# Kernel tuning notes

Measured on AMD Instinct MI355X. Metric: run time of the kernel, lower is better.

Reference implementation:

```python
import jax, jax.numpy as jnp
import numpy as np

IGST = 10      # ghost-cell width (module-level constant in the source)
EPS = 0.01     # tol passed to NeuralODE -> runge_kutta eps
W_SCALE = 0.05 # keep the learned stencil contractive over 100 steps


def cal_boundry(u):
    # Replace the IGST ghost cells on each side with the nearest interior value.
    m, n, l = u.shape
    left = jnp.broadcast_to(u[:, :, IGST:IGST + 1], (m, n, IGST))
    right = jnp.broadcast_to(u[:, :, -IGST - 1:-IGST], (m, n, IGST))
    return jnp.concatenate([left, u[:, :, IGST:-IGST], right], axis=2)


def stencil_f(z, W):
    # func: learned 1D stencil = same-padded conv over the spatial axis.
    # z: [m, n, l], W: [n_out, n_in, k]
    return jax.lax.conv_general_dilated(
        z, W, window_strides=(1,), padding='SAME',
        dimension_numbers=('NCH', 'OIH', 'NCH'))


def setup_inputs() -> dict:
    key = jax.random.key(0)
    k1, k2 = jax.random.split(key)
    z0 = jax.random.normal(k1, (32, 16, 8192), dtype=jnp.float32)
    W = jax.random.normal(k2, (16, 16, 5), dtype=jnp.float32) * W_SCALE
    return {'z0': z0, 'W': W, 't1_t0': 1}


def reference(z0, W, t1_t0):
    # SSP-RK3 (Shu-Osher) explicit time stepping with ghost-cell BCs.
    n_steps = int(round(t1_t0 / EPS))
    h = t1_t0 / n_steps

    def step(z, _):
        k1 = cal_boundry(z + h * stencil_f(z, W))
        k2 = cal_boundry(0.75 * z + 0.25 * k1 + 0.25 * h * stencil_f(k1, W))
        z_new = cal_boundry(z / 3.0 + 2.0 * k2 / 3.0 + 2.0 * h * stencil_f(k2, W) / 3.0)
        return z_new, None

    z, _ = jax.lax.scan(step, z0, None, length=n_steps)
    return z
```

## Files before the change

kernel.cpp:

```cpp
#include <hip/hip_runtime.h>


#define NCH    16
#define LL     8192
#define TX     128
#define NBX    64
#define NB     32
#define NSTEPS 100
#define SPK    5
#define NKER   (NSTEPS / SPK)

#define RAD    30
#define NCHUNK 31
#define ISLAB  190

#define WCOLS  96
#define DWIN   1072
#define NROWS  592
#define NMT    37
#define NKC    34
#define XSTR   1096

typedef __bf16 bf16x8 __attribute__((ext_vector_type(8)));
typedef __bf16 bf16x4 __attribute__((ext_vector_type(4)));
typedef float  f32x4  __attribute__((ext_vector_type(4)));

__device__ __align__(16) float g_G [ 5*256];
__device__ __align__(16) float g_G2[ 9*256];
__device__ __align__(16) float g_Tp[13*256];
__device__ __align__(16) float g_T2[25*256];
__device__ __align__(16) float g_T3[37*256];
__device__ __align__(16) float g_T4[49*256];
__device__ __align__(16) float g_T5[61*256];
__device__ __align__(16) __bf16 g_Sfrag[NCHUNK*64*8];
__device__ __align__(16) float g_CL[(size_t)NROWS*DWIN];
__device__ __align__(16) float g_CR[(size_t)NROWS*DWIN];
__device__ __align__(16) __bf16 g_Cpack[2][NMT][NKC][512];

__global__ void build_G(const float* __restrict__ W, const int* __restrict__ tptr) {
  const float h = (float)(*tptr) / (float)NSTEPS;
  const int o = threadIdx.x >> 4, i = threadIdx.x & 15;
#pragma unroll
  for (int k = 0; k < 5; ++k)
    g_G[k*256 + o*16 + i] = h * W[o*80 + i*5 + k];
}

__global__ void compose_k(int mode) {
  const float* A; int ra; const float* B; int rb; float* C;
  switch (mode) {
    case 0:  A = g_G;  ra = 2;  B = g_G;  rb = 2; C = g_G2; break;
    case 1:  A = g_G2; ra = 4;  B = g_G;  rb = 2; C = g_Tp; break;
    case 2:  A = g_Tp; ra = 6;  B = g_Tp; rb = 6; C = g_T2; break;
    case 3:  A = g_T2; ra = 12; B = g_Tp; rb = 6; C = g_T3; break;
    case 4:  A = g_T3; ra = 18; B = g_Tp; rb = 6; C = g_T4; break;
    default: A = g_T4; ra = 24; B = g_Tp; rb = 6; C = g_T5; break;
  }
  const int rc = ra + rb;
  const int d = (int)blockIdx.x - rc;
  const int o = threadIdx.x >> 4, i = threadIdx.x & 15;
  float acc = 0.f;
  for (int a = -ra; a <= ra; ++a) {
    const int b = d - a;
    if (b < -rb || b > rb) continue;
    const float* Am = A + (a+ra)*256 + o*16;
    const float* Bm = B + (b+rb)*256 + i;
#pragma unroll
    for (int j = 0; j < 16; ++j) acc += Am[j] * Bm[j*16];
  }
  C[(size_t)blockIdx.x*256 + o*16 + i] = acc;
}

__global__ void build_Tp() {
  const int o = threadIdx.x >> 4, i = threadIdx.x & 15;
#pragma unroll
  for (int k = 0; k < 13; ++k) {
    const int d = k - 6;
    float v = g_Tp[k*256 + o*16 + i] * (1.f/6.f);
    if (d >= -4 && d <= 4) v += 0.5f * g_G2[(d+4)*256 + o*16 + i];
    if (d >= -2 && d <= 2) v += g_G[(d+2)*256 + o*16 + i];
    g_Tp[k*256 + o*16 + i] = v;
  }
}

__device__ __forceinline__ float padread(const float* M, int r, int d, int oi) {
  return (d >= -r && d <= r) ? M[(d+r)*256 + oi] : 0.f;
}

__global__ void pack_S() {
  const int c = blockIdx.x;
  const int lane = threadIdx.x & 63;
  const int jj = (threadIdx.x >> 6) * 2;
  const int gg = lane >> 4, n = lane & 15;
  const int k = 2*c + (gg >> 1);
  const int d = k - RAD;
#pragma unroll
  for (int u = 0; u < 2; ++u) {
    const int j = jj + u;
    const int i = (gg & 1)*8 + j;
    const int oi = n*16 + i;
    float v = 0.f;
    if (k <= 60) {
      v = 5.f  * padread(g_Tp,  6, d, oi)
        + 10.f * padread(g_T2, 12, d, oi)
        + 10.f * padread(g_T3, 18, d, oi)
        + 5.f  * padread(g_T4, 24, d, oi)
        +        padread(g_T5, 30, d, oi);
    }
    g_Sfrag[((size_t)c*64 + lane)*8 + j] = (__bf16)v;
  }
}

__global__ void pack_C() {
  const int mt = blockIdx.x, e = blockIdx.y;
  const float* __restrict__ C = e ? g_CR : g_CL;
  __bf16* __restrict__ P = &g_Cpack[e][mt][0][0];
  for (int idx = threadIdx.x; idx < NKC * 512; idx += 256) {
    const int kc = idx >> 9, q = idx & 511;
    const int ln = q >> 3, j = q & 7;
    const int k = kc * 32 + (ln >> 4) * 8 + j;
    const int row = mt * 16 + (ln & 15);
    P[idx] = (__bf16)((k < DWIN) ? C[(size_t)row * DWIN + k] : 0.f);
  }
}

__device__ __forceinline__ int ldsIdx(int col, int ch) {
  return col * NCH + (ch ^ ((col & 4) << 1));
}

__device__ __forceinline__ bf16x8 mkA(const float* __restrict__ W, int c, int g, int n) {
  const int kk = c * 2 + (g >> 1);
  bf16x8 a;
#pragma unroll
  for (int j = 0; j < 8; ++j) {
    const int i = (g & 1) * 8 + j;
    a[j] = (__bf16)((kk < 5) ? W[n * (NCH * 5) + i * 5 + kk] : 0.0f);
  }
  return a;
}

__global__ __launch_bounds__(384)
void edge_evolve(const float* __restrict__ W, const int* __restrict__ tptr) {
  __shared__ __align__(16) __bf16 ES[2][WCOLS * NCH];
  const int j = blockIdx.x, e = blockIdx.y;
  const float h = (float)(*tptr) / (float)NSTEPS;
  const int tid = threadIdx.x, lane = tid & 63, wv = tid >> 6;
  const int g = lane >> 4, n = lane & 15;
  const int t = wv, mycol = 16 * t + n;
  const int cwj = (e ? 29 : 0) + (j >> 4), chj = j & 15;

  const bf16x8 af0 = mkA(W, 0, g, n);
  const bf16x8 af1 = mkA(W, 1, g, n);
  const bf16x8 af2 = mkA(W, 2, g, n);

  const int hot = ldsIdx(cwj, chj);
  for (int q = tid; q < WCOLS * NCH; q += 384)
    ES[0][q] = (__bf16)(q == hot ? 1.f : 0.f);

  f32x4 kz = {0.f, 0.f, 0.f, 0.f};
  if (mycol == cwj && g == (chj >> 2)) kz[chj & 3] = 1.f;
  f32x4 kf = {0.f, 0.f, 0.f, 0.f};
  __syncthreads();

  const float c13 = 1.0f / 3.0f, c23 = 2.0f / 3.0f;
  int rb = 0;
#pragma unroll 1
  for (int sp = 0; sp < SPK; ++sp) {
#pragma unroll 1
    for (int st = 0; st < 3; ++st) {
      const float az  = (st == 0) ? 1.0f : (st == 1) ? 0.75f : c13;
      const float ak  = (st == 0) ? 0.0f : (st == 1) ? 0.25f : c23;
      const float agh = (st == 0) ? h    : (st == 1) ? 0.25f*h : c23*h;
      const __bf16* RS = ES[rb];
      __bf16* WS = ES[rb ^ 1];
      f32x4 acc = {0.f, 0.f, 0.f, 0.f};
#pragma unroll
      for (int c = 0; c < 3; ++c) {
        const int kk = c * 2 + (g >> 1);
        int s = mycol + kk - 2;
        s = min(max(s, 0), WCOLS - 1);
        const bf16x8 bfrag = *(const bf16x8*)(&RS[ldsIdx(s, (g & 1) * 8)]);
        const bf16x8 a = (c == 0) ? af0 : (c == 1) ? af1 : af2;
        acc = __builtin_amdgcn_mfma_f32_16x16x32_bf16(a, bfrag, acc, 0, 0, 0);
      }
      f32x4 v;
#pragma unroll
      for (int r = 0; r < 4; ++r) v[r] = az * kz[r] + ak * kf[r] + agh * acc[r];
      if (e == 0 && t == 0) {
#pragma unroll
        for (int r = 0; r < 4; ++r) {
          const float sv = __shfl(v[r], (lane & 48) | 10, 64);
          if (n < 10) v[r] = sv;
        }
      }
      if (e == 1 && t == 5) {
#pragma unroll
        for (int r = 0; r < 4; ++r) {
          const float sv = __shfl(v[r], (lane & 48) | 5, 64);
          if (n > 5) v[r] = sv;
        }
      }
      kf = v;
      if (st == 2) kz = v;
      bf16x4 bv = { (__bf16)v[0], (__bf16)v[1], (__bf16)v[2], (__bf16)v[3] };
      *(bf16x4*)(&WS[ldsIdx(mycol, g * 4)]) = bv;
      __syncthreads();
      rb ^= 1;
    }
  }

  if (e == 0) {
    if (mycol <= 36) {
      const int rowb = mycol * 16 + g * 4;
#pragma unroll
      for (int r = 0; r < 4; ++r) {
        const float id = (mycol == cwj && (g * 4 + r) == chj) ? 1.f : 0.f;
        g_CL[(size_t)(rowb + r) * DWIN + j] = kz[r] - id;
      }
    }
  } else {
    if (mycol >= 59) {
      const int rowb = (mycol - 59) * 16 + g * 4;
#pragma unroll
      for (int r = 0; r < 4; ++r) {
        const float id = (mycol == cwj && (g * 4 + r) == chj) ? 1.f : 0.f;
        g_CR[(size_t)(rowb + r) * DWIN + j] = kz[r] - id;
      }
    }
  }
}

__global__ __launch_bounds__(256) void transpose_kernel(const float* __restrict__ in,
                                                        float* __restrict__ out) {
  const int b = blockIdx.y;
  const int x = blockIdx.x * 256 + threadIdx.x;
  const float* __restrict__ ib = in + (size_t)b * NCH * LL;
  float* __restrict__ ob = out + (size_t)b * NCH * LL;
  float v[NCH];
#pragma unroll
  for (int c = 0; c < NCH; ++c) v[c] = ib[c * LL + x];
#pragma unroll
  for (int c = 0; c < NCH; c += 4)
    *(float4*)(ob + (size_t)x * NCH + c) = make_float4(v[c], v[c+1], v[c+2], v[c+3]);
}

__global__ __launch_bounds__(256)
void multistep_kernel(
    const float* __restrict__ zin,
    float* __restrict__ zout,
    const int* __restrict__ tptr, int finalKer)
{
  __shared__ __align__(16) char SMEM[16 * XSTR * 2];

  const int b = blockIdx.y, bx = blockIdx.x;
  const int tid = threadIdx.x, lane = tid & 63, wv = tid >> 6;
  const int g = lane >> 4, n = lane & 15;

  if (bx < NBX) {
    __bf16* __restrict__ ISL = (__bf16*)SMEM;
    const float* __restrict__ zb = zin + (size_t)b * NCH * LL;
    float* __restrict__ ob = zout + (size_t)b * NCH * LL;
    const int x0 = bx * TX;
    const bool leftE = (bx == 0), rightE = (bx == NBX - 1);

    for (int q = tid; q < ISLAB * 4; q += 256) {
      const int s = q >> 2, cg = (q & 3) * 4;
      int gx = x0 - RAD + s;
      gx = min(max(gx, 0), LL - 1);
      const float4 v = *(const float4*)(zb + (size_t)gx * NCH + cg);
      bf16x4 bv = { (__bf16)v.x, (__bf16)v.y, (__bf16)v.z, (__bf16)v.w };
      *(bf16x4*)(&ISL[ldsIdx(s, cg)]) = bv;
    }

    const int o0 = 16 * wv + n;
    const f32x4 kz0 = *(const f32x4*)(zb + (size_t)(x0 + o0) * NCH + g * 4);
    const f32x4 kz1 = *(const f32x4*)(zb + (size_t)(x0 + o0 + 64) * NCH + g * 4);
    __syncthreads();

    const int p = g >> 1, hsel = g & 1;
    f32x4 acc0 = {0.f,0.f,0.f,0.f}, acc1 = acc0;
    const __bf16* Af = g_Sfrag + (size_t)lane * 8;
    int col0 = o0 + p;
#pragma unroll
    for (int c = 0; c < NCHUNK; ++c) {
      const bf16x8 a = *(const bf16x8*)(Af + (size_t)c * 512);
      const int xr = ((((col0 >> 2) & 1) ^ hsel) << 4);
      const bf16x8 b0 = *(const bf16x8*)((const char*)ISL + col0 * 32 + xr);
      const bf16x8 b1 = *(const bf16x8*)((const char*)ISL + (col0 + 64) * 32 + xr);
      acc0 = __builtin_amdgcn_mfma_f32_16x16x32_bf16(a, b0, acc0, 0, 0, 0);
      acc1 = __builtin_amdgcn_mfma_f32_16x16x32_bf16(a, b1, acc1, 0, 0, 0);
      col0 += 2;
    }

    f32x4 v0, v1;
#pragma unroll
    for (int r = 0; r < 4; ++r) { v0[r] = kz0[r] + acc0[r]; v1[r] = kz1[r] + acc1[r]; }

    const bool st0 = !(leftE && o0 <= 36);
    const bool st1 = !(rightE && o0 >= 27);
    if (!finalKer) {
      if (st0) *(f32x4*)(ob + (size_t)(x0 + o0) * NCH + g * 4) = v0;
      if (st1) *(f32x4*)(ob + (size_t)(x0 + o0 + 64) * NCH + g * 4) = v1;
    } else {
#pragma unroll
      for (int r = 0; r < 4; ++r) {
        if (st0) ob[(size_t)(g * 4 + r) * LL + (x0 + o0)] = v0[r];
        if (st1) ob[(size_t)(g * 4 + r) * LL + (x0 + o0 + 64)] = v1[r];
      }
    }
  } else {
    const int rid = b;
    const int side = rid & 1, bhalf = (rid >> 1) & 1, mseg = rid >> 2;
    __bf16* __restrict__ XL = (__bf16*)SMEM;
    const size_t woff = side ? (size_t)(LL - 67) * NCH : 0;

    for (int q = tid; q < 16 * 268; q += 256) {
      const int bb = q / 268, c4 = q % 268;
      const f32x4 v = *(const f32x4*)(zin + (size_t)(bhalf*16 + bb) * NCH * LL
                                      + woff + c4 * 4);
      bf16x4 bv = { (__bf16)v[0], (__bf16)v[1], (__bf16)v[2], (__bf16)v[3] };
      *(bf16x4*)(&XL[bb * XSTR + c4 * 4]) = bv;
    }
    for (int q = tid; q < 16 * 16; q += 256)
      XL[(q >> 4) * XSTR + 1072 + (q & 15)] = (__bf16)0.f;
    __syncthreads();

    const int q = mseg * 4 + wv;
    const int mt0 = q, mt1 = q + 32;
    const bool has1 = (mt1 < NMT);
    f32x4 acc0 = {0.f,0.f,0.f,0.f}, acc1 = acc0;
    const __bf16* __restrict__ Cp = &g_Cpack[side][0][0][0];
    const __bf16* __restrict__ Xr = &XL[n * XSTR + g * 8];

#pragma unroll 2
    for (int kc = 0; kc < NKC; ++kc) {
      const bf16x8 a = *(const bf16x8*)(Xr + kc * 32);
      const bf16x8 b0 = *(const bf16x8*)(Cp + ((size_t)mt0 * NKC + kc) * 512 + lane * 8);
      acc0 = __builtin_amdgcn_mfma_f32_16x16x32_bf16(a, b0, acc0, 0, 0, 0);
      if (has1) {
        const bf16x8 b1 = *(const bf16x8*)(Cp + ((size_t)mt1 * NKC + kc) * 512 + lane * 8);
        acc1 = __builtin_amdgcn_mfma_f32_16x16x32_bf16(a, b1, acc1, 0, 0, 0);
      }
    }

#pragma unroll
    for (int i = 0; i < 2; ++i) {
      if (i == 1 && !has1) break;
      const int mt = i ? mt1 : mt0;
      const f32x4 acc = i ? acc1 : acc0;
      const int x = side ? (LL - 37 + mt) : mt;
#pragma unroll
      for (int r = 0; r < 4; ++r) {
        const int bb = bhalf * 16 + 4 * g + r;
        const size_t base = (size_t)bb * NCH * LL;
        const float ov = zin[base + (size_t)x * NCH + n] + acc[r];
        if (!finalKer) zout[base + (size_t)x * NCH + n] = ov;
        else           zout[base + (size_t)n * LL + x] = ov;
      }
    }
  }
}

extern "C" void kernel_launch(void* const* d_in, const int* in_sizes, int n_in,
                              void* d_out, int out_size, void* d_ws, size_t ws_size,
                              hipStream_t stream) {
  const float* z0 = (const float*)d_in[0];
  const float* W  = (const float*)d_in[1];
  const int*   t  = (const int*)d_in[2];

  float* Q = (float*)d_out;
  float* P = (float*)d_ws;

  build_G<<<dim3(1), dim3(256), 0, stream>>>(W, t);
  compose_k<<<dim3( 9), dim3(256), 0, stream>>>(0);
  compose_k<<<dim3(13), dim3(256), 0, stream>>>(1);
  build_Tp<<<dim3(1), dim3(256), 0, stream>>>();
  compose_k<<<dim3(25), dim3(256), 0, stream>>>(2);
  compose_k<<<dim3(37), dim3(256), 0, stream>>>(3);
  compose_k<<<dim3(49), dim3(256), 0, stream>>>(4);
  compose_k<<<dim3(61), dim3(256), 0, stream>>>(5);
  pack_S<<<dim3(NCHUNK), dim3(256), 0, stream>>>();

  edge_evolve<<<dim3(DWIN, 2), dim3(384), 0, stream>>>(W, t);
  pack_C<<<dim3(NMT, 2), dim3(256), 0, stream>>>();

  dim3 block(256);
  transpose_kernel<<<dim3(32, NB), block, 0, stream>>>(z0, Q);

  dim3 mgrid(NBX + 1, NB);
  for (int k = 1; k <= NKER; ++k) {
    if (k & 1) multistep_kernel<<<mgrid, block, 0, stream>>>(Q, P, t, 0);
    else       multistep_kernel<<<mgrid, block, 0, stream>>>(P, Q, t, k == NKER);
  }
}
```

Baseline: 789.2 us.

## Fuse setup kernels, single-wave edge evolve, split boundary blocks finer

Merges the chain of small stencil-composition and packing kernels into one 1024-thread block, removing eight launches and their serialization. Rewrites edge_evolve to use one wavefront per block that loops over six column tiles, keeping kz/kf state in LDS so no block barriers are needed. Splits the boundary-correction work of the multistep kernel across an extra grid column with 8-batch groups, which halves LDS per block and spreads the edge GEMM over more blocks. In exchange, half of each MFMA's A rows are zero-padded, so those lanes do wasted work.

```diff
diff --git a/kernel.cpp b/kernel.cpp
--- a/kernel.cpp
+++ b/kernel.cpp
@@ -37,48 +37,23 @@
 __device__ __align__(16) float g_CR[(size_t)NROWS*DWIN];
 __device__ __align__(16) __bf16 g_Cpack[2][NMT][NKC][512];
 
-__global__ void build_G(const float* __restrict__ W, const int* __restrict__ tptr) {
-  const float h = (float)(*tptr) / (float)NSTEPS;
-  const int o = threadIdx.x >> 4, i = threadIdx.x & 15;
-#pragma unroll
-  for (int k = 0; k < 5; ++k)
-    g_G[k*256 + o*16 + i] = h * W[o*80 + i*5 + k];
-}
-
-__global__ void compose_k(int mode) {
-  const float* A; int ra; const float* B; int rb; float* C;
-  switch (mode) {
-    case 0:  A = g_G;  ra = 2;  B = g_G;  rb = 2; C = g_G2; break;
-    case 1:  A = g_G2; ra = 4;  B = g_G;  rb = 2; C = g_Tp; break;
-    case 2:  A = g_Tp; ra = 6;  B = g_Tp; rb = 6; C = g_T2; break;
-    case 3:  A = g_T2; ra = 12; B = g_Tp; rb = 6; C = g_T3; break;
-    case 4:  A = g_T3; ra = 18; B = g_Tp; rb = 6; C = g_T4; break;
-    default: A = g_T4; ra = 24; B = g_Tp; rb = 6; C = g_T5; break;
-  }
-  const int rc = ra + rb;
-  const int d = (int)blockIdx.x - rc;
-  const int o = threadIdx.x >> 4, i = threadIdx.x & 15;
-  float acc = 0.f;
-  for (int a = -ra; a <= ra; ++a) {
-    const int b = d - a;
-    if (b < -rb || b > rb) continue;
-    const float* Am = A + (a+ra)*256 + o*16;
-    const float* Bm = B + (b+rb)*256 + i;
-#pragma unroll
-    for (int j = 0; j < 16; ++j) acc += Am[j] * Bm[j*16];
-  }
-  C[(size_t)blockIdx.x*256 + o*16 + i] = acc;
-}
-
-__global__ void build_Tp() {
-  const int o = threadIdx.x >> 4, i = threadIdx.x & 15;
-#pragma unroll
-  for (int k = 0; k < 13; ++k) {
-    const int d = k - 6;
-    float v = g_Tp[k*256 + o*16 + i] * (1.f/6.f);
-    if (d >= -4 && d <= 4) v += 0.5f * g_G2[(d+4)*256 + o*16 + i];
-    if (d >= -2 && d <= 2) v += g_G[(d+2)*256 + o*16 + i];
-    g_Tp[k*256 + o*16 + i] = v;
+__device__ __forceinline__ void composeSeg(const float* __restrict__ A, int ra,
+                                           const float* __restrict__ B, int rb,
+                                           float* __restrict__ C, int q, int oi) {
+  const int o = oi >> 4, i = oi & 15;
+  const int rc = ra + rb, nt = 2*rc + 1;
+  for (int kt = q; kt < nt; kt += 4) {
+    const int d = kt - rc;
+    float acc = 0.f;
+    for (int a = -ra; a <= ra; ++a) {
+      const int b = d - a;
+      if (b < -rb || b > rb) continue;
+      const float* Am = A + (a+ra)*256 + o*16;
+      const float* Bm = B + (b+rb)*256 + i;
+#pragma unroll
+      for (int j = 0; j < 16; ++j) acc += Am[j] * Bm[j*16];
+    }
+    C[(size_t)kt*256 + oi] = acc;
   }
 }
 
@@ -86,25 +61,46 @@
   return (d >= -r && d <= r) ? M[(d+r)*256 + oi] : 0.f;
 }
 
-__global__ void pack_S() {
-  const int c = blockIdx.x;
-  const int lane = threadIdx.x & 63;
-  const int jj = (threadIdx.x >> 6) * 2;
-  const int gg = lane >> 4, n = lane & 15;
-  const int k = 2*c + (gg >> 1);
-  const int d = k - RAD;
-#pragma unroll
-  for (int u = 0; u < 2; ++u) {
-    const int j = jj + u;
-    const int i = (gg & 1)*8 + j;
-    const int oi = n*16 + i;
+__global__ __launch_bounds__(1024)
+void setup_S(const float* __restrict__ W, const int* __restrict__ tptr) {
+  const float h = (float)(*tptr) / (float)NSTEPS;
+  const int q = threadIdx.x >> 8;
+  const int oi = threadIdx.x & 255;
+  const int o = oi >> 4, i = oi & 15;
+
+  for (int k = q; k < 5; k += 4)
+    g_G[k*256 + oi] = h * W[o*80 + i*5 + k];
+  __syncthreads();
+  composeSeg(g_G,  2, g_G,  2, g_G2, q, oi);  __syncthreads();
+  composeSeg(g_G2, 4, g_G,  2, g_Tp, q, oi);  __syncthreads();
+  for (int k = q; k < 13; k += 4) {
+    const int d = k - 6;
+    float v = g_Tp[k*256 + oi] * (1.f/6.f);
+    if (d >= -4 && d <= 4) v += 0.5f * g_G2[(d+4)*256 + oi];
+    if (d >= -2 && d <= 2) v += g_G[(d+2)*256 + oi];
+    g_Tp[k*256 + oi] = v;
+  }
+  __syncthreads();
+  composeSeg(g_Tp, 6,  g_Tp, 6, g_T2, q, oi); __syncthreads();
+  composeSeg(g_T2, 12, g_Tp, 6, g_T3, q, oi); __syncthreads();
+  composeSeg(g_T3, 18, g_Tp, 6, g_T4, q, oi); __syncthreads();
+  composeSeg(g_T4, 24, g_Tp, 6, g_T5, q, oi); __syncthreads();
+
+  for (int idx = threadIdx.x; idx < NCHUNK*512; idx += 1024) {
+    const int c = idx >> 9, rest = idx & 511;
+    const int lane = rest >> 3, j = rest & 7;
+    const int gg = lane >> 4, n = lane & 15;
+    const int k = 2*c + (gg >> 1);
+    const int d = k - RAD;
+    const int ii = (gg & 1)*8 + j;
+    const int oi2 = n*16 + ii;
     float v = 0.f;
     if (k <= 60) {
-      v = 5.f  * padread(g_Tp,  6, d, oi)
-        + 10.f * padread(g_T2, 12, d, oi)
-        + 10.f * padread(g_T3, 18, d, oi)
-        + 5.f  * padread(g_T4, 24, d, oi)
-        +        padread(g_T5, 30, d, oi);
+      v = 5.f  * padread(g_Tp,  6, d, oi2)
+        + 10.f * padread(g_T2, 12, d, oi2)
+        + 10.f * padread(g_T3, 18, d, oi2)
+        + 5.f  * padread(g_T4, 24, d, oi2)
+        +        padread(g_T5, 30, d, oi2);
     }
     g_Sfrag[((size_t)c*64 + lane)*8 + j] = (__bf16)v;
   }
@@ -138,14 +134,15 @@
   return a;
 }
 
-__global__ __launch_bounds__(384)
+__global__ __launch_bounds__(64)
 void edge_evolve(const float* __restrict__ W, const int* __restrict__ tptr) {
   __shared__ __align__(16) __bf16 ES[2][WCOLS * NCH];
+  __shared__ __align__(16) float  KZ[WCOLS * NCH];
+  __shared__ __align__(16) float  KF[WCOLS * NCH];
   const int j = blockIdx.x, e = blockIdx.y;
   const float h = (float)(*tptr) / (float)NSTEPS;
-  const int tid = threadIdx.x, lane = tid & 63, wv = tid >> 6;
+  const int lane = threadIdx.x;
   const int g = lane >> 4, n = lane & 15;
-  const int t = wv, mycol = 16 * t + n;
   const int cwj = (e ? 29 : 0) + (j >> 4), chj = j & 15;
 
   const bf16x8 af0 = mkA(W, 0, g, n);
@@ -153,13 +150,12 @@
   const bf16x8 af2 = mkA(W, 2, g, n);
 
   const int hot = ldsIdx(cwj, chj);
-  for (int q = tid; q < WCOLS * NCH; q += 384)
+  const int hotz = cwj * 16 + chj;
+  for (int q = lane; q < WCOLS * NCH; q += 64) {
     ES[0][q] = (__bf16)(q == hot ? 1.f : 0.f);
-
-  f32x4 kz = {0.f, 0.f, 0.f, 0.f};
-  if (mycol == cwj && g == (chj >> 2)) kz[chj & 3] = 1.f;
-  f32x4 kf = {0.f, 0.f, 0.f, 0.f};
-  __syncthreads();
+    KZ[q] = (q == hotz) ? 1.f : 0.f;
+    KF[q] = 0.f;
+  }
 
   const float c13 = 1.0f / 3.0f, c23 = 2.0f / 3.0f;
   int rb = 0;
@@ -172,59 +168,58 @@
       const float agh = (st == 0) ? h    : (st == 1) ? 0.25f*h : c23*h;
       const __bf16* RS = ES[rb];
       __bf16* WS = ES[rb ^ 1];
-      f32x4 acc = {0.f, 0.f, 0.f, 0.f};
-#pragma unroll
-      for (int c = 0; c < 3; ++c) {
-        const int kk = c * 2 + (g >> 1);
-        int s = mycol + kk - 2;
-        s = min(max(s, 0), WCOLS - 1);
-        const bf16x8 bfrag = *(const bf16x8*)(&RS[ldsIdx(s, (g & 1) * 8)]);
-        const bf16x8 a = (c == 0) ? af0 : (c == 1) ? af1 : af2;
-        acc = __builtin_amdgcn_mfma_f32_16x16x32_bf16(a, bfrag, acc, 0, 0, 0);
-      }
-      f32x4 v;
-#pragma unroll
-      for (int r = 0; r < 4; ++r) v[r] = az * kz[r] + ak * kf[r] + agh * acc[r];
-      if (e == 0 && t == 0) {
-#pragma unroll
-        for (int r = 0; r < 4; ++r) {
-          const float sv = __shfl(v[r], (lane & 48) | 10, 64);
-          if (n < 10) v[r] = sv;
+#pragma unroll
+      for (int t = 0; t < 6; ++t) {
+        const int mycol = 16 * t + n;
+        const f32x4 kz = *(const f32x4*)(&KZ[mycol * 16 + g * 4]);
+        const f32x4 kf = *(const f32x4*)(&KF[mycol * 16 + g * 4]);
+        f32x4 acc = {0.f, 0.f, 0.f, 0.f};
+#pragma unroll
+        for (int c = 0; c < 3; ++c) {
+          const int kk = c * 2 + (g >> 1);
+          int s = mycol + kk - 2;
+          s = min(max(s, 0), WCOLS - 1);
+          const bf16x8 bfrag = *(const bf16x8*)(&RS[ldsIdx(s, (g & 1) * 8)]);
+          const bf16x8 a = (c == 0) ? af0 : (c == 1) ? af1 : af2;
+          acc = __builtin_amdgcn_mfma_f32_16x16x32_bf16(a, bfrag, acc, 0, 0, 0);
         }
-      }
-      if (e == 1 && t == 5) {
-#pragma unroll
-        for (int r = 0; r < 4; ++r) {
-          const float sv = __shfl(v[r], (lane & 48) | 5, 64);
-          if (n > 5) v[r] = sv;
+        f32x4 v;
+#pragma unroll
+        for (int r = 0; r < 4; ++r) v[r] = az * kz[r] + ak * kf[r] + agh * acc[r];
+        if (e == 0 && t == 0) {
+#pragma unroll
+          for (int r = 0; r < 4; ++r) {
+            const float sv = __shfl(v[r], (lane & 48) | 10, 64);
+            if (n < 10) v[r] = sv;
+          }
         }
-      }
-      kf = v;
-      if (st == 2) kz = v;
-      bf16x4 bv = { (__bf16)v[0], (__bf16)v[1], (__bf16)v[2], (__bf16)v[3] };
-      *(bf16x4*)(&WS[ldsIdx(mycol, g * 4)]) = bv;
-      __syncthreads();
+        if (e == 1 && t == 5) {
+#pragma unroll
+          for (int r = 0; r < 4; ++r) {
+            const float sv = __shfl(v[r], (lane & 48) | 5, 64);
+            if (n > 5) v[r] = sv;
+          }
+        }
+        *(f32x4*)(&KF[mycol * 16 + g * 4]) = v;
+        if (st == 2) *(f32x4*)(&KZ[mycol * 16 + g * 4]) = v;
+        bf16x4 bv = { (__bf16)v[0], (__bf16)v[1], (__bf16)v[2], (__bf16)v[3] };
+        *(bf16x4*)(&WS[ldsIdx(mycol, g * 4)]) = bv;
+      }
       rb ^= 1;
     }
   }
 
   if (e == 0) {
-    if (mycol <= 36) {
-      const int rowb = mycol * 16 + g * 4;
-#pragma unroll
-      for (int r = 0; r < 4; ++r) {
-        const float id = (mycol == cwj && (g * 4 + r) == chj) ? 1.f : 0.f;
-        g_CL[(size_t)(rowb + r) * DWIN + j] = kz[r] - id;
-      }
+    for (int idx = lane; idx < NROWS; idx += 64) {
+      const int col = idx >> 4, ch = idx & 15;
+      const float id = (col == cwj && ch == chj) ? 1.f : 0.f;
+      g_CL[(size_t)idx * DWIN + j] = KZ[col * 16 + ch] - id;
     }
   } else {
-    if (mycol >= 59) {
-      const int rowb = (mycol - 59) * 16 + g * 4;
-#pragma unroll
-      for (int r = 0; r < 4; ++r) {
-        const float id = (mycol == cwj && (g * 4 + r) == chj) ? 1.f : 0.f;
-        g_CR[(size_t)(rowb + r) * DWIN + j] = kz[r] - id;
-      }
+    for (int idx = lane; idx < NROWS; idx += 64) {
+      const int col = 59 + (idx >> 4), ch = idx & 15;
+      const float id = (col == cwj && ch == chj) ? 1.f : 0.f;
+      g_CR[(size_t)idx * DWIN + j] = KZ[col * 16 + ch] - id;
     }
   }
 }
@@ -249,7 +244,7 @@
     float* __restrict__ zout,
     const int* __restrict__ tptr, int finalKer)
 {
-  __shared__ __align__(16) char SMEM[16 * XSTR * 2];
+  __shared__ __align__(16) char SMEM[8 * XSTR * 2];
 
   const int b = blockIdx.y, bx = blockIdx.x;
   const int tid = threadIdx.x, lane = tid & 63, wv = tid >> 6;
@@ -308,32 +303,37 @@
       }
     }
   } else {
-    const int rid = b;
-    const int side = rid & 1, bhalf = (rid >> 1) & 1, mseg = rid >> 2;
+    const int rid = (bx - NBX) * NB + b;
+    const int side = rid & 1, bgroup = (rid >> 1) & 3, mseg = rid >> 3;
     __bf16* __restrict__ XL = (__bf16*)SMEM;
     const size_t woff = side ? (size_t)(LL - 67) * NCH : 0;
 
-    for (int q = tid; q < 16 * 268; q += 256) {
+    for (int q = tid; q < 8 * 268; q += 256) {
       const int bb = q / 268, c4 = q % 268;
-      const f32x4 v = *(const f32x4*)(zin + (size_t)(bhalf*16 + bb) * NCH * LL
+      const f32x4 v = *(const f32x4*)(zin + (size_t)(bgroup*8 + bb) * NCH * LL
                                       + woff + c4 * 4);
       bf16x4 bv = { (__bf16)v[0], (__bf16)v[1], (__bf16)v[2], (__bf16)v[3] };
       *(bf16x4*)(&XL[bb * XSTR + c4 * 4]) = bv;
     }
-    for (int q = tid; q < 16 * 16; q += 256)
-      XL[(q >> 4) * XSTR + 1072 + (q & 15)] = (__bf16)0.f;
+    if (tid < 8 * 24)
+      XL[(tid / 24) * XSTR + 1072 + (tid % 24)] = (__bf16)0.f;
     __syncthreads();
 
-    const int q = mseg * 4 + wv;
-    const int mt0 = q, mt1 = q + 32;
-    const bool has1 = (mt1 < NMT);
+    const int mt0 = mseg + 8 * wv;
+    const int mt1 = mseg + 32;
+    const bool has1 = (wv == 0 && mt1 < NMT);
     f32x4 acc0 = {0.f,0.f,0.f,0.f}, acc1 = acc0;
     const __bf16* __restrict__ Cp = &g_Cpack[side][0][0][0];
-    const __bf16* __restrict__ Xr = &XL[n * XSTR + g * 8];
+    const __bf16* __restrict__ Xr = &XL[(n & 7) * XSTR + g * 8];
 
 #pragma unroll 2
     for (int kc = 0; kc < NKC; ++kc) {
-      const bf16x8 a = *(const bf16x8*)(Xr + kc * 32);
+      bf16x8 a;
+      if (n < 8) a = *(const bf16x8*)(Xr + kc * 32);
+      else {
+#pragma unroll
+        for (int j = 0; j < 8; ++j) a[j] = (__bf16)0.f;
+      }
       const bf16x8 b0 = *(const bf16x8*)(Cp + ((size_t)mt0 * NKC + kc) * 512 + lane * 8);
       acc0 = __builtin_amdgcn_mfma_f32_16x16x32_bf16(a, b0, acc0, 0, 0, 0);
       if (has1) {
@@ -348,13 +348,15 @@
       const int mt = i ? mt1 : mt0;
       const f32x4 acc = i ? acc1 : acc0;
       const int x = side ? (LL - 37 + mt) : mt;
-#pragma unroll
-      for (int r = 0; r < 4; ++r) {
-        const int bb = bhalf * 16 + 4 * g + r;
-        const size_t base = (size_t)bb * NCH * LL;
-        const float ov = zin[base + (size_t)x * NCH + n] + acc[r];
-        if (!finalKer) zout[base + (size_t)x * NCH + n] = ov;
-        else           zout[base + (size_t)n * LL + x] = ov;
+      if (g < 2) {
+#pragma unroll
+        for (int r = 0; r < 4; ++r) {
+          const int bb = bgroup * 8 + 4 * g + r;
+          const size_t base = (size_t)bb * NCH * LL;
+          const float ov = zin[base + (size_t)x * NCH + n] + acc[r];
+          if (!finalKer) zout[base + (size_t)x * NCH + n] = ov;
+          else           zout[base + (size_t)n * LL + x] = ov;
+        }
       }
     }
   }
@@ -370,23 +372,14 @@
   float* Q = (float*)d_out;
   float* P = (float*)d_ws;
 
-  build_G<<<dim3(1), dim3(256), 0, stream>>>(W, t);
-  compose_k<<<dim3( 9), dim3(256), 0, stream>>>(0);
-  compose_k<<<dim3(13), dim3(256), 0, stream>>>(1);
-  build_Tp<<<dim3(1), dim3(256), 0, stream>>>();
-  compose_k<<<dim3(25), dim3(256), 0, stream>>>(2);
-  compose_k<<<dim3(37), dim3(256), 0, stream>>>(3);
-  compose_k<<<dim3(49), dim3(256), 0, stream>>>(4);
-  compose_k<<<dim3(61), dim3(256), 0, stream>>>(5);
-  pack_S<<<dim3(NCHUNK), dim3(256), 0, stream>>>();
-
-  edge_evolve<<<dim3(DWIN, 2), dim3(384), 0, stream>>>(W, t);
+  setup_S<<<dim3(1), dim3(1024), 0, stream>>>(W, t);
+  edge_evolve<<<dim3(DWIN, 2), dim3(64), 0, stream>>>(W, t);
   pack_C<<<dim3(NMT, 2), dim3(256), 0, stream>>>();
 
   dim3 block(256);
   transpose_kernel<<<dim3(32, NB), block, 0, stream>>>(z0, Q);
 
-  dim3 mgrid(NBX + 1, NB);
+  dim3 mgrid(NBX + 2, NB);
   for (int k = 1; k <= NKER; ++k) {
     if (k & 1) multistep_kernel<<<mgrid, block, 0, stream>>>(Q, P, t, 0);
     else       multistep_kernel<<<mgrid, block, 0, stream>>>(P, Q, t, k == NKER);
```

After: 1.219 ms. +54.5%, slower.
